# Performance work log

Hardware: AMD Instinct MI355X
Metric: run time of the kernel (lower is better)

Reference implementation:

```python
import jax, jax.numpy as jnp
import numpy as np

H = 128  # h_size


def setup_inputs() -> dict:
    key = jax.random.key(0)
    ks = jax.random.split(key, 6)
    depth, n_trees = 16, 4
    N = 2 ** depth - 1          # nodes per complete binary tree
    T = n_trees * N             # total nodes
    return {
        "iou": jax.random.normal(ks[0], (T, 3 * H), dtype=jnp.float32),
        "h": jax.random.normal(ks[1], (T, H), dtype=jnp.float32),
        "c": jax.random.normal(ks[2], (T, H), dtype=jnp.float32),
        "W_iou": jax.random.normal(ks[3], (3 * H, 2 * H), dtype=jnp.float32) * 0.05,
        "b_iou": jnp.zeros((3 * H,), dtype=jnp.float32),
        "W_f": jax.random.normal(ks[4], (2 * H, 2 * H), dtype=jnp.float32) * 0.05,
        "b_f": jnp.zeros((2 * H,), dtype=jnp.float32),
        "depth": depth,
        "n_trees": n_trees,
    }


def _gates(iou, b_iou):
    i, o, u = jnp.split(iou + b_iou, 3, axis=1)
    return jax.nn.sigmoid(i), jax.nn.sigmoid(o), jnp.tanh(u)


def reference(iou, h, c, W_iou, b_iou, W_f, b_f, depth, n_trees):
    N = 2 ** depth - 1
    offs = (jnp.arange(n_trees) * N)[:, None]  # per-tree node offsets

    # --- leaf frontier: no messages -> apply_node_func only (keeps initial iou, c) ---
    l = depth - 1
    idx = (offs + jnp.arange(2 ** l - 1, 2 ** (l + 1) - 1)[None, :]).reshape(-1)
    i, o, u = _gates(iou[idx], b_iou)
    c_new = i * u + c[idx]
    h = h.at[idx].set(o * jnp.tanh(c_new))
    c = c.at[idx].set(c_new)

    # --- internal levels, bottom-up (level-parallel topological propagation) ---
    for l in range(depth - 2, -1, -1):
        loc = jnp.arange(2 ** l - 1, 2 ** (l + 1) - 1)
        idx = (offs + loc[None, :]).reshape(-1)
        lidx = (offs + (2 * loc + 1)[None, :]).reshape(-1)  # left child
        ridx = lidx + 1                                      # right child
        # reduce_func: gather children, forget gates, sum-reduce c, new iou
        h_cat = jnp.concatenate([h[lidx], h[ridx]], axis=-1)          # [n, 2H]
        f = jax.nn.sigmoid(h_cat @ W_f.T + b_f).reshape(-1, 2, H)     # [n, 2, H]
        c_kids = jnp.stack([c[lidx], c[ridx]], axis=1)                # [n, 2, H]
        c_red = jnp.sum(f * c_kids, axis=1)                           # [n, H]
        iou_red = h_cat @ W_iou.T                                     # [n, 3H]
        # apply_node_func
        i, o, u = _gates(iou_red, b_iou)
        c_new = i * u + c_red
        h = h.at[idx].set(o * jnp.tanh(c_new))
        c = c.at[idx].set(c_new)
    return h
```

## Files before the change

### kernel.cpp

```cpp
#include <hip/hip_runtime.h>

#define HH   128
#define H2   256
#define H3   384
#define NPT  65535
#define TPB  512

typedef __bf16    bf16x8 __attribute__((ext_vector_type(8)));
typedef float     f32x4  __attribute__((ext_vector_type(4)));
typedef _Float16  f16x4  __attribute__((ext_vector_type(4)));
typedef _Float16  half_t;

__device__ unsigned short Wb_g[640 * 256];

__device__ __forceinline__ float fsig(float x)  { return 1.0f / (1.0f + __expf(-x)); }
__device__ __forceinline__ float ftanh(float x) { return 1.0f - 2.0f / (__expf(2.0f * x) + 1.0f); }
__device__ __forceinline__ unsigned short f2bf(float f) {
    unsigned u = __float_as_uint(f);
    u += 0x7fffu + ((u >> 16) & 1u);
    return (unsigned short)(u >> 16);
}
__device__ __forceinline__ int swz(int off) { return off ^ (((off >> 9) & 7) << 4); }

__global__ __launch_bounds__(256) void conv_k(const float* __restrict__ W_iou,
                                              const float* __restrict__ W_f)
{
    int t    = blockIdx.x * 256 + threadIdx.x;
    int base = t * 4;
    int j = base >> 8, k = base & 255;
    const float* src = (j < H3) ? (W_iou + j * H2 + k)
                                : (W_f + (j - H3) * H2 + k);
    float4 v = *(const float4*)src;
    ushort4 p;
    p.x = f2bf(v.x); p.y = f2bf(v.y); p.z = f2bf(v.z); p.w = f2bf(v.w);
    *(ushort4*)(Wb_g + base) = p;
}

#define GATES5(PI, PO, PU, PL, PR, CL, CR, HV, CV) \
    { CV = fsig(PI) * ftanh(PU) + fsig(PL) * (CL) + fsig(PR) * (CR); \
      HV = fsig(PO) * ftanh(CV); }

__global__ __launch_bounds__(TPB, 4) void leaf14_k(
    const float* __restrict__ iou, const float* __restrict__ c_in,
    const float* __restrict__ b_iou, const float* __restrict__ b_f,
    float* __restrict__ h_g, half_t* __restrict__ c_ws,
    unsigned short* __restrict__ h_bf)
{
    __shared__ __align__(16) unsigned short A_lds[32 * H2];
    __shared__ __align__(16) half_t         C_lds[64 * HH];

    const int tid = threadIdx.x;
    const int w  = tid >> 6;
    const int lr = tid & 15;
    const int lc = (tid & 63) >> 4;
    const int ee = w * 16 + lr;
    const int nb = gridDim.x;
    const int bs = (blockIdx.x & 7) * (nb >> 3) + (blockIdx.x >> 3);
    const int node0 = bs * 32;
    const int tree  = node0 >> 14;
    const int lbase = tree * NPT + 32767 + 2 * (node0 & 16383);

#pragma unroll
    for (int it = 0; it < 4; ++it) {
        int p   = tid + TPB * it;
        int row = p >> 5;
        int e4  = p & 31;
        int grow = lbase + row;
        const float* ip = iou + (size_t)grow * H3 + e4 * 4;
        f32x4 vi = __builtin_nontemporal_load((const f32x4*)(ip));
        f32x4 vo = __builtin_nontemporal_load((const f32x4*)(ip + HH));
        f32x4 vu = __builtin_nontemporal_load((const f32x4*)(ip + 2 * HH));
        f32x4 vc = __builtin_nontemporal_load((const f32x4*)(c_in + (size_t)grow * HH + e4 * 4));
        float4 bi4 = *(const float4*)(b_iou + e4 * 4);
        float4 bo4 = *(const float4*)(b_iou + HH + e4 * 4);
        float4 bu4 = *(const float4*)(b_iou + 2 * HH + e4 * 4);

        f32x4 hn, cn;
#define DOL(X) { float iv = fsig(vi.X + bi4.X); float ov = fsig(vo.X + bo4.X); \
                 float uv = ftanh(vu.X + bu4.X); float cv = iv * uv + vc.X;    \
                 cn.X = cv; hn.X = ov * ftanh(cv); }
        DOL(x) DOL(y) DOL(z) DOL(w)
#undef DOL
        __builtin_nontemporal_store(hn, (f32x4*)(h_g + (size_t)grow * HH + e4 * 4));
        f16x4 cf; cf.x = (half_t)cn.x; cf.y = (half_t)cn.y;
        cf.z = (half_t)cn.z; cf.w = (half_t)cn.w;
        *(f16x4*)(C_lds + row * HH + e4 * 4) = cf;
        int m = row >> 1, half = row & 1;
        uint2 pk;
        pk.x = (unsigned)f2bf(hn.x) | ((unsigned)f2bf(hn.y) << 16);
        pk.y = (unsigned)f2bf(hn.z) | ((unsigned)f2bf(hn.w) << 16);
        int byte = (m * 512 + half * 256 + e4 * 8) ^ ((m & 7) << 4);
        *(uint2*)((char*)A_lds + byte) = pk;
    }
    __syncthreads();

    f32x4 acc[2][5] = {};
    const unsigned short* Wp = Wb_g + ee * H2 + lc * 8;
#pragma unroll
    for (int kk = 0; kk < 8; ++kk) {
        bf16x8 a0 = *(const bf16x8*)((const char*)A_lds + swz(lr * 512 + kk * 64 + lc * 16));
        bf16x8 a1 = *(const bf16x8*)((const char*)A_lds + swz((16 + lr) * 512 + kk * 64 + lc * 16));
#pragma unroll
        for (int g = 0; g < 5; ++g) {
            bf16x8 b = *(const bf16x8*)(Wp + g * HH * H2 + kk * 32);
            acc[0][g] = __builtin_amdgcn_mfma_f32_16x16x32_bf16(a0, b, acc[0][g], 0, 0, 0);
            acc[1][g] = __builtin_amdgcn_mfma_f32_16x16x32_bf16(a1, b, acc[1][g], 0, 0, 0);
        }
    }

    const float bi = b_iou[ee], bo = b_iou[HH + ee], bu = b_iou[2 * HH + ee];
    const float bl = b_f[ee],   br = b_f[HH + ee];
#pragma unroll
    for (int mt = 0; mt < 2; ++mt)
#pragma unroll
        for (int r = 0; r < 4; ++r) {
            int q    = mt * 16 + lc * 4 + r;
            int node = node0 + q;
            int base = tree * NPT + 16383 + (node & 16383);
            int o    = base * HH + ee;
            float cl = (float)C_lds[(2 * q) * HH + ee];
            float cr = (float)C_lds[(2 * q + 1) * HH + ee];
            float hv, cv;
            GATES5(acc[mt][0][r] + bi, acc[mt][1][r] + bo, acc[mt][2][r] + bu,
                   acc[mt][3][r] + bl, acc[mt][4][r] + br, cl, cr, hv, cv);
            __builtin_nontemporal_store(hv, h_g + o);
            c_ws[o] = (half_t)cv;
            h_bf[o] = f2bf(hv);
        }
}

__global__ __launch_bounds__(TPB, 4) void level_k(
    int lvl,
    const float* __restrict__ b_iou, const float* __restrict__ b_f,
    float* __restrict__ h_g, half_t* __restrict__ c_ws,
    unsigned short* __restrict__ h_bf)
{
    __shared__ __align__(16) unsigned short A_lds[32 * H2];

    const int tid = threadIdx.x;
    const int w  = tid >> 6;
    const int lr = tid & 15;
    const int lc = (tid & 63) >> 4;
    const int ee = w * 16 + lr;
    const int nb = gridDim.x;
    const int bs = (nb >= 8) ? ((blockIdx.x & 7) * (nb >> 3) + (blockIdx.x >> 3))
                             : blockIdx.x;
    const int node0 = bs * 32;
    const int loc0  = (1 << lvl) - 1;
    const int lmask = loc0;

#pragma unroll
    for (int it = 0; it < 2; ++it) {
        int item = tid + TPB * it;
        int m = item >> 5, u = item & 31;
        int node = node0 + m;
        int tree = node >> lvl;
        int loc  = loc0 + (node & lmask);
        int coff = (tree * NPT + 2 * loc + 1 + (u >> 4)) * HH + (u & 15) * 8;
        uint4 v = *(const uint4*)(h_bf + coff);
        *(uint4*)((char*)A_lds + swz(m * 512 + u * 16)) = v;
    }
    __syncthreads();

    int   rofs[2][4];
    float clv[2][4], crv[2][4];
#pragma unroll
    for (int mt = 0; mt < 2; ++mt)
#pragma unroll
        for (int r = 0; r < 4; ++r) {
            int node = node0 + mt * 16 + lc * 4 + r;
            int tree = node >> lvl;
            int loc  = loc0 + (node & lmask);
            int base = tree * NPT + loc;
            int lrow = base + loc + 1;
            rofs[mt][r] = base * HH + ee;
            clv[mt][r] = (float)c_ws[lrow * HH + ee];
            crv[mt][r] = (float)c_ws[lrow * HH + HH + ee];
        }

    f32x4 acc[2][5] = {};
    const unsigned short* Wp = Wb_g + ee * H2 + lc * 8;
#pragma unroll
    for (int kk = 0; kk < 8; ++kk) {
        bf16x8 a0 = *(const bf16x8*)((const char*)A_lds + swz(lr * 512 + kk * 64 + lc * 16));
        bf16x8 a1 = *(const bf16x8*)((const char*)A_lds + swz((16 + lr) * 512 + kk * 64 + lc * 16));
#pragma unroll
        for (int g = 0; g < 5; ++g) {
            bf16x8 b = *(const bf16x8*)(Wp + g * HH * H2 + kk * 32);
            acc[0][g] = __builtin_amdgcn_mfma_f32_16x16x32_bf16(a0, b, acc[0][g], 0, 0, 0);
            acc[1][g] = __builtin_amdgcn_mfma_f32_16x16x32_bf16(a1, b, acc[1][g], 0, 0, 0);
        }
    }

    const float bi = b_iou[ee], bo = b_iou[HH + ee], bu = b_iou[2 * HH + ee];
    const float bl = b_f[ee],   br = b_f[HH + ee];
#pragma unroll
    for (int mt = 0; mt < 2; ++mt)
#pragma unroll
        for (int r = 0; r < 4; ++r) {
            float hv, cv;
            GATES5(acc[mt][0][r] + bi, acc[mt][1][r] + bo, acc[mt][2][r] + bu,
                   acc[mt][3][r] + bl, acc[mt][4][r] + br, clv[mt][r], crv[mt][r], hv, cv);
            int o = rofs[mt][r];
            __builtin_nontemporal_store(hv, h_g + o);
            c_ws[o] = (half_t)cv;
            h_bf[o] = f2bf(hv);
        }
}

__global__ __launch_bounds__(TPB, 2) void solo_k(
    const float* __restrict__ b_iou, const float* __restrict__ b_f,
    float* __restrict__ h_g, half_t* __restrict__ c_ws,
    const unsigned short* __restrict__ h_bf)
{
    __shared__ __align__(16) unsigned char hb[49152];

    const int tid = threadIdx.x;
    const int w = tid >> 6, lr = tid & 15, lc = (tid & 63) >> 4;
    const int ee = w * 16 + lr;
    const int tb = blockIdx.x * NPT;
    const float bi = b_iou[ee], bo = b_iou[HH + ee], bu = b_iou[2 * HH + ee];
    const float bl = b_f[ee],   br = b_f[HH + ee];

    bf16x8 Bf[5][8];
    const unsigned short* Wp = Wb_g + ee * H2 + lc * 8;
#pragma unroll
    for (int g = 0; g < 5; ++g)
#pragma unroll
        for (int kk = 0; kk < 8; ++kk)
            Bf[g][kk] = *(const bf16x8*)(Wp + g * HH * H2 + kk * 32);

#pragma unroll
    for (int it = 0; it < 4; ++it) {
        int p = tid + TPB * it;
        int cc = p >> 4, q = p & 15;
        uint4 v = *(const uint4*)(h_bf + (tb + 127 + cc) * HH + q * 8);
        *(uint4*)(hb + swz(p * 16)) = v;
    }
    __syncthreads();

#pragma unroll 1
    for (int tt = 0; tt < 2; ++tt) {
        f32x4 acc[2][5] = {};
#pragma unroll
        for (int kk = 0; kk < 8; ++kk) {
            bf16x8 a0 = *(const bf16x8*)(hb + swz(tt * 16384 + lr * 512 + kk * 64 + lc * 16));
            bf16x8 a1 = *(const bf16x8*)(hb + swz(tt * 16384 + (16 + lr) * 512 + kk * 64 + lc * 16));
#pragma unroll
            for (int g = 0; g < 5; ++g) {
                acc[0][g] = __builtin_amdgcn_mfma_f32_16x16x32_bf16(a0, Bf[g][kk], acc[0][g], 0, 0, 0);
                acc[1][g] = __builtin_amdgcn_mfma_f32_16x16x32_bf16(a1, Bf[g][kk], acc[1][g], 0, 0, 0);
            }
        }
#pragma unroll
        for (int mt = 0; mt < 2; ++mt)
#pragma unroll
            for (int r = 0; r < 4; ++r) {
                int j    = tt * 32 + mt * 16 + lc * 4 + r;
                int row  = tb + 63 + j;
                int lrow = tb + 127 + 2 * j;
                float cl = (float)c_ws[lrow * HH + ee];
                float cr = (float)c_ws[lrow * HH + HH + ee];
                float hv, cv;
                GATES5(acc[mt][0][r] + bi, acc[mt][1][r] + bo, acc[mt][2][r] + bu,
                       acc[mt][3][r] + bl, acc[mt][4][r] + br, cl, cr, hv, cv);
                h_g[row * HH + ee]  = hv;
                c_ws[row * HH + ee] = (half_t)cv;
                *(unsigned short*)(hb + 32768 + swz(j * 256 + ee * 2)) = f2bf(hv);
            }
    }

#pragma unroll 1
    for (int l = 5; l >= 0; --l) {
        const int nl     = 1 << l;
        const int loc0   = nl - 1;
        const int cloc0  = 2 * nl - 1;
        const int cbase  = (l == 5) ? 32768 : ((l & 1) ? 16384 : 0);
        const int obase  = (l == 5) ? 0 : (((l & 1) ? 16384 : 0) ^ 16384);
        const bool mt1   = (nl > 16);

        __syncthreads();

        f32x4 acc[2][5] = {};
#pragma unroll
        for (int kk = 0; kk < 8; ++kk) {
            bf16x8 a0 = *(const bf16x8*)(hb + cbase + swz(lr * 512 + kk * 64 + lc * 16));
#pragma unroll
            for (int g = 0; g < 5; ++g)
                acc[0][g] = __builtin_amdgcn_mfma_f32_16x16x32_bf16(a0, Bf[g][kk], acc[0][g], 0, 0, 0);
            if (mt1) {
                bf16x8 a1 = *(const bf16x8*)(hb + cbase + swz((16 + lr) * 512 + kk * 64 + lc * 16));
#pragma unroll
                for (int g = 0; g < 5; ++g)
                    acc[1][g] = __builtin_amdgcn_mfma_f32_16x16x32_bf16(a1, Bf[g][kk], acc[1][g], 0, 0, 0);
            }
        }
        __syncthreads();

#pragma unroll
        for (int mt = 0; mt < 2; ++mt)
#pragma unroll
            for (int r = 0; r < 4; ++r) {
                int j = mt * 16 + lc * 4 + r;
                if (j >= nl) continue;
                int row  = tb + loc0 + j;
                int lrow = tb + cloc0 + 2 * j;
                float cl = (float)c_ws[lrow * HH + ee];
                float cr = (float)c_ws[lrow * HH + HH + ee];
                float hv, cv;
                GATES5(acc[mt][0][r] + bi, acc[mt][1][r] + bo, acc[mt][2][r] + bu,
                       acc[mt][3][r] + bl, acc[mt][4][r] + br, cl, cr, hv, cv);
                h_g[row * HH + ee]  = hv;
                c_ws[row * HH + ee] = (half_t)cv;
                *(unsigned short*)(hb + obase + swz(j * 256 + ee * 2)) = f2bf(hv);
            }
    }
}

extern "C" void kernel_launch(void* const* d_in, const int* in_sizes, int n_in,
                              void* d_out, int out_size, void* d_ws, size_t ws_size,
                              hipStream_t stream)
{
    const float* iou   = (const float*)d_in[0];
    const float* c_in  = (const float*)d_in[2];
    const float* W_iou = (const float*)d_in[3];
    const float* b_iou = (const float*)d_in[4];
    const float* W_f   = (const float*)d_in[5];
    const float* b_f   = (const float*)d_in[6];
    float* h_out = (float*)d_out;
    half_t* c_ws = (half_t*)d_ws;
    unsigned short* h_bf = (unsigned short*)((char*)d_ws + (size_t)72 * 1024 * 1024);

    conv_k<<<160, 256, 0, stream>>>(W_iou, W_f);
    leaf14_k<<<2048, TPB, 0, stream>>>(iou, c_in, b_iou, b_f, h_out, c_ws, h_bf);
    for (int l = 13; l >= 7; --l) {
        int blocks = (4 << l) / 32;
        level_k<<<blocks, TPB, 0, stream>>>(l, b_iou, b_f, h_out, c_ws, h_bf);
    }
    solo_k<<<4, TPB, 0, stream>>>(b_iou, b_f, h_out, c_ws, h_bf);
}
```

Baseline: 338.3 us.

## Fuse tree levels 10 through 7 into one kernel with shared-memory subtree

Replaces four separate per-level launches for levels 10 to 7 with one kernel. Each block processes a 32-node subtree slice and keeps the intermediate h (bf16) and c (fp16) in LDS between levels. Only the level-7 results go back to global memory for the final solo kernel, and the intermediate levels write only fp32 h. This removes launch overhead and the global round trips for intermediate state. In exchange, the later levels run with only 128 blocks and mostly idle MFMA rows, so much of the GPU sits unused.

```diff
diff --git a/kernel.cpp b/kernel.cpp
--- a/kernel.cpp
+++ b/kernel.cpp
@@ -208,6 +208,177 @@
         }
 }
 
+__global__ __launch_bounds__(TPB, 2) void quad_k(
+    const float* __restrict__ b_iou, const float* __restrict__ b_f,
+    float* __restrict__ h_g, half_t* __restrict__ c_ws,
+    unsigned short* __restrict__ h_bf)
+{
+    __shared__ __align__(16) unsigned short A10[32 * H2];
+    __shared__ __align__(16) unsigned short A9[16 * H2];
+    __shared__ __align__(16) unsigned short A8[16 * H2];
+    __shared__ __align__(16) unsigned short A7[16 * H2];
+    __shared__ __align__(16) half_t C10[32 * HH];
+    __shared__ __align__(16) half_t C9[16 * HH];
+    __shared__ __align__(16) half_t C8[8 * HH];
+
+    const int tid = threadIdx.x;
+    const int w  = tid >> 6;
+    const int lr = tid & 15;
+    const int lc = (tid & 63) >> 4;
+    const int ee = w * 16 + lr;
+    const int b  = blockIdx.x;
+    const float bi = b_iou[ee], bo = b_iou[HH + ee], bu = b_iou[2 * HH + ee];
+    const float bl = b_f[ee],   br = b_f[HH + ee];
+    const unsigned short* Wp = Wb_g + ee * H2 + lc * 8;
+
+    {
+        uint4 z = make_uint4(0u, 0u, 0u, 0u);
+        *(uint4*)((char*)A8 + tid * 16) = z;
+        *(uint4*)((char*)A7 + tid * 16) = z;
+    }
+#pragma unroll
+    for (int it = 0; it < 2; ++it) {
+        int item = tid + TPB * it;
+        int m = item >> 5, u = item & 31;
+        int node = b * 32 + m;
+        int tree = node >> 10;
+        int loc  = 1023 + (node & 1023);
+        int coff = (tree * NPT + 2 * loc + 1 + (u >> 4)) * HH + (u & 15) * 8;
+        uint4 v = *(const uint4*)(h_bf + coff);
+        *(uint4*)((char*)A10 + swz(m * 512 + u * 16)) = v;
+    }
+    __syncthreads();
+
+    {
+        f32x4 acc[2][5] = {};
+#pragma unroll
+        for (int kk = 0; kk < 8; ++kk) {
+            bf16x8 a0 = *(const bf16x8*)((const char*)A10 + swz(lr * 512 + kk * 64 + lc * 16));
+            bf16x8 a1 = *(const bf16x8*)((const char*)A10 + swz((16 + lr) * 512 + kk * 64 + lc * 16));
+#pragma unroll
+            for (int g = 0; g < 5; ++g) {
+                bf16x8 bb = *(const bf16x8*)(Wp + g * HH * H2 + kk * 32);
+                acc[0][g] = __builtin_amdgcn_mfma_f32_16x16x32_bf16(a0, bb, acc[0][g], 0, 0, 0);
+                acc[1][g] = __builtin_amdgcn_mfma_f32_16x16x32_bf16(a1, bb, acc[1][g], 0, 0, 0);
+            }
+        }
+#pragma unroll
+        for (int mt = 0; mt < 2; ++mt)
+#pragma unroll
+            for (int r = 0; r < 4; ++r) {
+                int q    = mt * 16 + lc * 4 + r;
+                int node = b * 32 + q;
+                int tree = node >> 10;
+                int loc  = 1023 + (node & 1023);
+                int base = tree * NPT + loc;
+                int lrow = base + loc + 1;
+                float cl = (float)c_ws[lrow * HH + ee];
+                float cr = (float)c_ws[lrow * HH + HH + ee];
+                float hv, cv;
+                GATES5(acc[mt][0][r] + bi, acc[mt][1][r] + bo, acc[mt][2][r] + bu,
+                       acc[mt][3][r] + bl, acc[mt][4][r] + br, cl, cr, hv, cv);
+                __builtin_nontemporal_store(hv, h_g + base * HH + ee);
+                int m = q >> 1, half = q & 1;
+                *(unsigned short*)((char*)A9 + ((m * 512 + half * 256 + ee * 2) ^ ((m & 7) << 4))) = f2bf(hv);
+                C10[q * HH + ee] = (half_t)cv;
+            }
+    }
+    __syncthreads();
+
+    {
+        f32x4 acc[5] = {};
+#pragma unroll
+        for (int kk = 0; kk < 8; ++kk) {
+            bf16x8 a0 = *(const bf16x8*)((const char*)A9 + swz(lr * 512 + kk * 64 + lc * 16));
+#pragma unroll
+            for (int g = 0; g < 5; ++g)
+                acc[g] = __builtin_amdgcn_mfma_f32_16x16x32_bf16(a0,
+                          *(const bf16x8*)(Wp + g * HH * H2 + kk * 32), acc[g], 0, 0, 0);
+        }
+#pragma unroll
+        for (int r = 0; r < 4; ++r) {
+            int j    = lc * 4 + r;
+            int node = b * 16 + j;
+            int tree = node >> 9;
+            int loc  = 511 + (node & 511);
+            int base = tree * NPT + loc;
+            float cl = (float)C10[(2 * j) * HH + ee];
+            float cr = (float)C10[(2 * j + 1) * HH + ee];
+            float hv, cv;
+            GATES5(acc[0][r] + bi, acc[1][r] + bo, acc[2][r] + bu,
+                   acc[3][r] + bl, acc[4][r] + br, cl, cr, hv, cv);
+            __builtin_nontemporal_store(hv, h_g + base * HH + ee);
+            int m = j >> 1, half = j & 1;
+            *(unsigned short*)((char*)A8 + ((m * 512 + half * 256 + ee * 2) ^ ((m & 7) << 4))) = f2bf(hv);
+            C9[j * HH + ee] = (half_t)cv;
+        }
+    }
+    __syncthreads();
+
+    {
+        f32x4 acc[5] = {};
+#pragma unroll
+        for (int kk = 0; kk < 8; ++kk) {
+            bf16x8 a0 = *(const bf16x8*)((const char*)A8 + swz(lr * 512 + kk * 64 + lc * 16));
+#pragma unroll
+            for (int g = 0; g < 5; ++g)
+                acc[g] = __builtin_amdgcn_mfma_f32_16x16x32_bf16(a0,
+                          *(const bf16x8*)(Wp + g * HH * H2 + kk * 32), acc[g], 0, 0, 0);
+        }
+#pragma unroll
+        for (int r = 0; r < 4; ++r) {
+            int j = lc * 4 + r;
+            if (j < 8) {
+                int node = b * 8 + j;
+                int tree = node >> 8;
+                int loc  = 255 + (node & 255);
+                int base = tree * NPT + loc;
+                float cl = (float)C9[(2 * j) * HH + ee];
+                float cr = (float)C9[(2 * j + 1) * HH + ee];
+                float hv, cv;
+                GATES5(acc[0][r] + bi, acc[1][r] + bo, acc[2][r] + bu,
+                       acc[3][r] + bl, acc[4][r] + br, cl, cr, hv, cv);
+                __builtin_nontemporal_store(hv, h_g + base * HH + ee);
+                int m = j >> 1, half = j & 1;
+                *(unsigned short*)((char*)A7 + ((m * 512 + half * 256 + ee * 2) ^ ((m & 7) << 4))) = f2bf(hv);
+                C8[j * HH + ee] = (half_t)cv;
+            }
+        }
+    }
+    __syncthreads();
+
+    {
+        f32x4 acc[5] = {};
+#pragma unroll
+        for (int kk = 0; kk < 8; ++kk) {
+            bf16x8 a0 = *(const bf16x8*)((const char*)A7 + swz(lr * 512 + kk * 64 + lc * 16));
+#pragma unroll
+            for (int g = 0; g < 5; ++g)
+                acc[g] = __builtin_amdgcn_mfma_f32_16x16x32_bf16(a0,
+                          *(const bf16x8*)(Wp + g * HH * H2 + kk * 32), acc[g], 0, 0, 0);
+        }
+#pragma unroll
+        for (int r = 0; r < 4; ++r) {
+            int j = lc * 4 + r;
+            if (j < 4) {
+                int node = b * 4 + j;
+                int tree = node >> 7;
+                int loc  = 127 + (node & 127);
+                int base = tree * NPT + loc;
+                int o    = base * HH + ee;
+                float cl = (float)C8[(2 * j) * HH + ee];
+                float cr = (float)C8[(2 * j + 1) * HH + ee];
+                float hv, cv;
+                GATES5(acc[0][r] + bi, acc[1][r] + bo, acc[2][r] + bu,
+                       acc[3][r] + bl, acc[4][r] + br, cl, cr, hv, cv);
+                h_g[o]  = hv;
+                c_ws[o] = (half_t)cv;
+                h_bf[o] = f2bf(hv);
+            }
+        }
+    }
+}
+
 __global__ __launch_bounds__(TPB, 2) void solo_k(
     const float* __restrict__ b_iou, const float* __restrict__ b_f,
     float* __restrict__ h_g, half_t* __restrict__ c_ws,
@@ -333,9 +504,10 @@
 
     conv_k<<<160, 256, 0, stream>>>(W_iou, W_f);
     leaf14_k<<<2048, TPB, 0, stream>>>(iou, c_in, b_iou, b_f, h_out, c_ws, h_bf);
-    for (int l = 13; l >= 7; --l) {
+    for (int l = 13; l >= 11; --l) {
         int blocks = (4 << l) / 32;
         level_k<<<blocks, TPB, 0, stream>>>(l, b_iou, b_f, h_out, c_ws, h_bf);
     }
+    quad_k<<<128, TPB, 0, stream>>>(b_iou, b_f, h_out, c_ws, h_bf);
     solo_k<<<4, TPB, 0, stream>>>(b_iou, b_f, h_out, c_ws, h_bf);
 }
```

New measurement: 326.9 us. -3.4%, faster.
